# Performance work log

Hardware: AMD Instinct MI355X
Metric: run time of the kernel (lower is better)

## Reference

```python
import jax, jax.numpy as jnp
import numpy as np

EMBED_DIM = 1024
LN_EPS = 1e-5


def _layernorm(x, w, b):
    m = jnp.mean(x, axis=-1, keepdims=True)
    v = jnp.mean(jnp.square(x - m), axis=-1, keepdims=True)
    return (x - m) * jax.lax.rsqrt(v + LN_EPS) * w + b


def _attention(q, k, v, scale):
    # q: [b, sq, d], k/v: [b, sk, d]
    scores = jnp.einsum('bqd,bkd->bqk', q, k) * scale
    probs = jax.nn.softmax(scores, axis=-1)
    return jnp.einsum('bqk,bkd->bqd', probs, v)


def setup_inputs() -> dict:
    key = jax.random.key(0)
    ks = jax.random.split(key, 16)
    B, SQ, SK, D, H = 8, 577, 13271, EMBED_DIM, 4  # H=int(4.0) per source
    return {
        'input_features': jax.random.normal(ks[0], (B, SK, D), jnp.float32),
        'query_feature': jax.random.normal(ks[1], (B, SQ, D), jnp.float32),
        'norm1_w': jax.random.uniform(ks[2], (D,), jnp.float32, 0.5, 1.5),
        'norm1_b': jax.random.normal(ks[3], (D,), jnp.float32) * 0.1,
        'norm2_w': jax.random.uniform(ks[4], (D,), jnp.float32, 0.5, 1.5),
        'norm2_b': jax.random.normal(ks[5], (D,), jnp.float32) * 0.1,
        'norm3_w': jax.random.uniform(ks[6], (D,), jnp.float32, 0.5, 1.5),
        'norm3_b': jax.random.normal(ks[7], (D,), jnp.float32) * 0.1,
        'gamma1': jax.random.uniform(ks[8], (D,), jnp.float32, 0.5, 1.5),
        'gamma2': jax.random.uniform(ks[9], (D,), jnp.float32, 0.5, 1.5),
        'fc1_w': jax.random.normal(ks[10], (H, D), jnp.float32) * (1.0 / np.sqrt(D)),
        'fc1_b': jax.random.normal(ks[11], (H,), jnp.float32) * 0.01,
        'fc2_w': jax.random.normal(ks[12], (D, H), jnp.float32) * (1.0 / np.sqrt(H)),
        'fc2_b': jax.random.normal(ks[13], (D,), jnp.float32) * 0.01,
    }


def reference(input_features, query_feature, norm1_w, norm1_b, norm2_w, norm2_b,
              norm3_w, norm3_b, gamma1, gamma2, fc1_w, fc1_b, fc2_w, fc2_b):
    scale = EMBED_DIM ** (-0.5)
    norm_X = _layernorm(input_features, norm1_w, norm1_b)
    norm_F_L = _layernorm(query_feature, norm2_w, norm2_b)
    # cross attention: query = last-layer feats, key/value = concat of earlier layers
    attended = _attention(norm_F_L, norm_X, norm_X, scale)
    # MLP with exact-erf GELU (torch nn.GELU default), dropout=0 -> identity
    h = jax.nn.gelu(attended @ fc1_w.T + fc1_b, approximate=False)
    cross_attended = h @ fc2_w.T + fc2_b
    norm_cross = _layernorm(cross_attended, norm3_w, norm3_b)
    self_attended = _attention(norm_cross, norm_cross, norm_cross, scale)
    skip_connect = cross_attended + gamma1 * self_attended
    return norm_F_L + gamma2 * skip_connect
```

## Files before the change

### kernel.cpp

```cpp
#include <hip/hip_runtime.h>
#include <hip/hip_bf16.h>
#include <math.h>

typedef unsigned short u16;
typedef __attribute__((ext_vector_type(4))) unsigned short u16x4;
typedef __attribute__((ext_vector_type(8))) __bf16 bf16x8;
typedef __attribute__((ext_vector_type(4))) float fx4;

#define DEV __device__ __forceinline__

DEV u16 f2bf(float f) {
    unsigned u = __float_as_uint(f);
    u += 0x7fffu + ((u >> 16) & 1u);
    return (u16)(u >> 16);
}

DEV void async_load16(const void* g, void* l) {
    __builtin_amdgcn_global_load_lds(
        (const __attribute__((address_space(1))) void*)g,
        (__attribute__((address_space(3))) void*)l, 16, 0, 0);
}

DEV void block_reduce2(float& a, float& b) {
    #pragma unroll
    for (int o = 32; o; o >>= 1) { a += __shfl_xor(a, o); b += __shfl_xor(b, o); }
    __shared__ float sa[4], sb[4];
    const int lane = threadIdx.x & 63, wv = threadIdx.x >> 6;
    if (lane == 0) { sa[wv] = a; sb[wv] = b; }
    __syncthreads();
    a = sa[0] + sa[1] + sa[2] + sa[3];
    b = sb[0] + sb[1] + sb[2] + sb[3];
    __syncthreads();
}

DEV void xcd_swizzle3(int& bx, int& by, int& bz) {
    const int nx = gridDim.x, ny = gridDim.y;
    const int total = nx * ny * gridDim.z;
    const int lin = blockIdx.x + nx * (blockIdx.y + ny * blockIdx.z);
    const int cpx = total >> 3;
    const int swz = (lin & 7) * cpx + (lin >> 3);
    bx = swz % nx;
    const int r = swz / nx;
    by = r % ny;
    bz = r / ny;
}

__global__ __launch_bounds__(256) void ln_k(
    const float* __restrict__ in, int rows_real,
    const float* __restrict__ w, const float* __restrict__ bias,
    u16* __restrict__ out_bf, float* __restrict__ out_f32, float out_scale)
{
    const int r = blockIdx.x, b = blockIdx.y, tid = threadIdx.x;
    const int rows_pad = gridDim.x;
    const size_t orow = ((size_t)b * rows_pad + r) * 1024 + tid * 4;
    if (r >= rows_real) {
        u16x4 z = {0, 0, 0, 0};
        *(u16x4*)&out_bf[orow] = z;
        if (out_f32) { fx4 zf = {0.f, 0.f, 0.f, 0.f}; *(fx4*)&out_f32[orow] = zf; }
        return;
    }
    const size_t irow = ((size_t)b * rows_real + r) * 1024 + tid * 4;
    fx4 x = *(const fx4*)&in[irow];
    float s1 = x.x + x.y + x.z + x.w;
    float s2 = x.x * x.x + x.y * x.y + x.z * x.z + x.w * x.w;
    block_reduce2(s1, s2);
    float m = s1 * (1.0f / 1024.0f);
    float var = s2 * (1.0f / 1024.0f) - m * m;
    float rs = rsqrtf(var + 1e-5f);
    fx4 wv4 = *(const fx4*)&w[tid * 4];
    fx4 bv4 = *(const fx4*)&bias[tid * 4];
    fx4 y;
    y.x = (x.x - m) * rs * wv4.x + bv4.x;
    y.y = (x.y - m) * rs * wv4.y + bv4.y;
    y.z = (x.z - m) * rs * wv4.z + bv4.z;
    y.w = (x.w - m) * rs * wv4.w + bv4.w;
    u16x4 o = { f2bf(y.x * out_scale), f2bf(y.y * out_scale),
                f2bf(y.z * out_scale), f2bf(y.w * out_scale) };
    *(u16x4*)&out_bf[orow] = o;
    if (out_f32) *(fx4*)&out_f32[orow] = y;
}

template<bool ATOMIC>
DEV void gemm_body(
    const u16* __restrict__ Ab, const u16* __restrict__ Bb, float* __restrict__ Cb,
    int k_begin, int iters, int lda, int ldb, int ldc)
{
    __shared__ u16 lA[2][128 * 32];
    __shared__ u16 lB[2][128 * 32];
    const int lane = threadIdx.x & 63, wv = threadIdx.x >> 6;
    const int wm = (wv >> 1) * 64, wn = (wv & 1) * 64;
    const int frow = lane & 15, quad = lane >> 4;

    fx4 acc[4][4];
    #pragma unroll
    for (int i = 0; i < 4; ++i)
        #pragma unroll
        for (int j = 0; j < 4; ++j) { acc[i][j].x = 0; acc[i][j].y = 0; acc[i][j].z = 0; acc[i][j].w = 0; }

    const int c0 = wv * 64 + lane;
    const int r0a = c0 >> 2, s0 = (c0 & 3) * 8;
    const int c1 = 256 + c0;
    const int r1a = c1 >> 2, s1 = (c1 & 3) * 8;

    auto stage = [&](int buf, int it) {
        const int k0 = k_begin + it * 32;
        async_load16(Ab + (size_t)r0a * lda + k0 + s0, &lA[buf][(wv * 64) * 8]);
        async_load16(Ab + (size_t)r1a * lda + k0 + s1, &lA[buf][(256 + wv * 64) * 8]);
        async_load16(Bb + (size_t)r0a * ldb + k0 + s0, &lB[buf][(wv * 64) * 8]);
        async_load16(Bb + (size_t)r1a * ldb + k0 + s1, &lB[buf][(256 + wv * 64) * 8]);
    };

    stage(0, 0);
    __syncthreads();
    int cur = 0;
    for (int it = 0; it < iters; ++it) {
        if (it + 1 < iters) stage(cur ^ 1, it + 1);
        bf16x8 af[4], bfr[4];
        #pragma unroll
        for (int i = 0; i < 4; ++i) {
            af[i]  = *(const bf16x8*)&lA[cur][(wm + i * 16 + frow) * 32 + quad * 8];
            bfr[i] = *(const bf16x8*)&lB[cur][(wn + i * 16 + frow) * 32 + quad * 8];
        }
        #pragma unroll
        for (int mi = 0; mi < 4; ++mi)
            #pragma unroll
            for (int ni = 0; ni < 4; ++ni)
                acc[mi][ni] = __builtin_amdgcn_mfma_f32_16x16x32_bf16(af[mi], bfr[ni], acc[mi][ni], 0, 0, 0);
        __syncthreads();
        cur ^= 1;
    }

    #pragma unroll
    for (int mi = 0; mi < 4; ++mi) {
        #pragma unroll
        for (int r = 0; r < 4; ++r) {
            const int row = wm + mi * 16 + quad * 4 + r;
            #pragma unroll
            for (int ni = 0; ni < 4; ++ni) {
                const int col = wn + ni * 16 + frow;
                if (ATOMIC) atomicAdd(&Cb[(size_t)row * ldc + col], acc[mi][ni][r]);
                else        __builtin_nontemporal_store(acc[mi][ni][r], &Cb[(size_t)row * ldc + col]);
            }
        }
    }
}

__global__ __launch_bounds__(256) void gemm_bt(
    const u16* __restrict__ A, const u16* __restrict__ B, float* __restrict__ C,
    int K, int lda, int ldb, int ldc, long As, long Bs, long Cs)
{
    const int bz = blockIdx.z;
    const u16* Ab = A + (size_t)bz * As + (size_t)blockIdx.y * 128 * lda;
    const u16* Bb = B + (size_t)bz * Bs + (size_t)blockIdx.x * 128 * ldb;
    float* Cb = C + (size_t)bz * Cs + (size_t)blockIdx.y * 128 * ldc + (size_t)blockIdx.x * 128;
    gemm_body<false>(Ab, Bb, Cb, 0, K / 32, lda, ldb, ldc);
}

template<int NS>
__global__ __launch_bounds__(256) void gemm_bt_sk(
    const u16* __restrict__ A, const u16* __restrict__ B, float* __restrict__ C,
    int iters_per, int lda, int ldb, int ldc, long As, long Bs, long Cs)
{
    int bx, by, bzz;
    xcd_swizzle3(bx, by, bzz);
    const int bz = bzz / NS, sp = bzz % NS;
    const u16* Ab = A + (size_t)bz * As + (size_t)by * 128 * lda;
    const u16* Bb = B + (size_t)bz * Bs + (size_t)bx * 128 * ldb;
    float* Cb = C + (size_t)bz * Cs + (size_t)by * 128 * ldc + (size_t)bx * 128;
    gemm_body<true>(Ab, Bb, Cb, sp * iters_per * 32, iters_per, lda, ldb, ldc);
}

template<int EPT4>
__global__ __launch_bounds__(256) void softmax_k(
    const float* __restrict__ S, u16* __restrict__ P,
    int n_real, int n_pad, float scale, long Ss, long Ps)
{
    const int tid = threadIdx.x;
    const float* Sr = S + (size_t)blockIdx.y * Ss + (size_t)blockIdx.x * n_pad;
    u16* Pr = P + (size_t)blockIdx.y * Ps + (size_t)blockIdx.x * n_pad;
    fx4 v[EPT4];
    float mx = -INFINITY;
    #pragma unroll
    for (int i = 0; i < EPT4; ++i) {
        const int base = (i * 256 + tid) * 4;
        fx4 s;
        if (base < n_pad) s = *(const fx4*)&Sr[base];
        else { s.x = -INFINITY; s.y = -INFINITY; s.z = -INFINITY; s.w = -INFINITY; }
        s.x = (base + 0 < n_real) ? s.x * scale : -INFINITY;
        s.y = (base + 1 < n_real) ? s.y * scale : -INFINITY;
        s.z = (base + 2 < n_real) ? s.z * scale : -INFINITY;
        s.w = (base + 3 < n_real) ? s.w * scale : -INFINITY;
        v[i] = s;
        mx = fmaxf(mx, fmaxf(fmaxf(s.x, s.y), fmaxf(s.z, s.w)));
    }
    #pragma unroll
    for (int o = 32; o; o >>= 1) mx = fmaxf(mx, __shfl_xor(mx, o));
    __shared__ float sm[4];
    const int lane = tid & 63, wvi = tid >> 6;
    if (lane == 0) sm[wvi] = mx;
    __syncthreads();
    mx = fmaxf(fmaxf(sm[0], sm[1]), fmaxf(sm[2], sm[3]));
    __syncthreads();
    float sum = 0.f;
    #pragma unroll
    for (int i = 0; i < EPT4; ++i) {
        fx4 e;
        e.x = __expf(v[i].x - mx); e.y = __expf(v[i].y - mx);
        e.z = __expf(v[i].z - mx); e.w = __expf(v[i].w - mx);
        v[i] = e;
        sum += e.x + e.y + e.z + e.w;
    }
    #pragma unroll
    for (int o = 32; o; o >>= 1) sum += __shfl_xor(sum, o);
    if (lane == 0) sm[wvi] = sum;
    __syncthreads();
    sum = sm[0] + sm[1] + sm[2] + sm[3];
    const float inv = 1.0f / sum;
    #pragma unroll
    for (int i = 0; i < EPT4; ++i) {
        const int base = (i * 256 + tid) * 4;
        if (base < n_pad) {
            u16x4 o = { f2bf(v[i].x * inv), f2bf(v[i].y * inv),
                        f2bf(v[i].z * inv), f2bf(v[i].w * inv) };
            *(u16x4*)&Pr[base] = o;
        }
    }
}

__global__ __launch_bounds__(256) void transpose_k(
    const u16* __restrict__ in, u16* __restrict__ out,
    int in_rows, int in_cols, long is, long os)
{
    __shared__ u16 t[64][68];
    const int b = blockIdx.z;
    const u16* I = in + (size_t)b * is;
    u16* O = out + (size_t)b * os;
    const int c0 = blockIdx.x * 64, r0 = blockIdx.y * 64;
    const int cx = threadIdx.x & 15, ry = threadIdx.x >> 4;
    u16x4 a[4];
    #pragma unroll
    for (int k = 0; k < 4; ++k)
        a[k] = *(const u16x4*)&I[(size_t)(r0 + 4 * ry + k) * in_cols + c0 + 4 * cx];
    #pragma unroll
    for (int e = 0; e < 4; ++e) {
        u16x4 o = { a[0][e], a[1][e], a[2][e], a[3][e] };
        *(u16x4*)&t[4 * cx + e][4 * ry] = o;
    }
    __syncthreads();
    #pragma unroll
    for (int k = 0; k < 4; ++k) {
        const int oc = 4 * ry + k;
        *(u16x4*)&O[(size_t)(c0 + oc) * in_rows + r0 + 4 * cx] =
            *(const u16x4*)&t[oc][4 * cx];
    }
}

__global__ __launch_bounds__(256) void mlp_ln_k(
    const float* __restrict__ att, const float* __restrict__ w1, const float* __restrict__ b1,
    const float* __restrict__ w2, const float* __restrict__ b2,
    const float* __restrict__ w3, const float* __restrict__ b3,
    float* __restrict__ ca, u16* __restrict__ nc, int rows_real)
{
    const int q = blockIdx.x, b = blockIdx.y, tid = threadIdx.x;
    const size_t row = ((size_t)b * gridDim.x + q) * 1024 + tid * 4;
    if (q >= rows_real) {
        fx4 zf = {0.f, 0.f, 0.f, 0.f}; u16x4 z = {0, 0, 0, 0};
        *(fx4*)&ca[row] = zf;
        *(u16x4*)&nc[row] = z;
        return;
    }
    fx4 x = *(const fx4*)&att[row];
    float p[4];
    #pragma unroll
    for (int j = 0; j < 4; ++j) {
        fx4 wj = *(const fx4*)&w1[j * 1024 + tid * 4];
        p[j] = x.x * wj.x + x.y * wj.y + x.z * wj.z + x.w * wj.w;
        #pragma unroll
        for (int o = 32; o; o >>= 1) p[j] += __shfl_xor(p[j], o);
    }
    __shared__ float sh[4][4];
    const int lane = tid & 63, wvi = tid >> 6;
    if (lane == 0) { sh[wvi][0] = p[0]; sh[wvi][1] = p[1]; sh[wvi][2] = p[2]; sh[wvi][3] = p[3]; }
    __syncthreads();
    float h[4];
    #pragma unroll
    for (int j = 0; j < 4; ++j) {
        float s = sh[0][j] + sh[1][j] + sh[2][j] + sh[3][j] + b1[j];
        h[j] = 0.5f * s * (1.0f + erff(s * 0.70710678118f));
    }
    float v[4]; float s1 = 0.f, s2 = 0.f;
    #pragma unroll
    for (int e = 0; e < 4; ++e) {
        const int d = tid * 4 + e;
        fx4 wd = *(const fx4*)&w2[d * 4];
        float t = h[0] * wd.x + h[1] * wd.y + h[2] * wd.z + h[3] * wd.w + b2[d];
        v[e] = t; s1 += t; s2 += t * t;
    }
    block_reduce2(s1, s2);
    const float m = s1 * (1.0f / 1024.0f);
    const float var = s2 * (1.0f / 1024.0f) - m * m;
    const float rs = rsqrtf(var + 1e-5f);
    fx4 cav = {v[0], v[1], v[2], v[3]};
    *(fx4*)&ca[row] = cav;
    fx4 w3v = *(const fx4*)&w3[tid * 4], b3v = *(const fx4*)&b3[tid * 4];
    u16x4 o = { f2bf((v[0] - m) * rs * w3v.x + b3v.x), f2bf((v[1] - m) * rs * w3v.y + b3v.y),
                f2bf((v[2] - m) * rs * w3v.z + b3v.z), f2bf((v[3] - m) * rs * w3v.w + b3v.w) };
    *(u16x4*)&nc[row] = o;
}

__global__ __launch_bounds__(256) void final_k(
    const float* __restrict__ nF, const float* __restrict__ ca,
    const float* __restrict__ att2, const float* __restrict__ g1,
    const float* __restrict__ g2, float* __restrict__ out, int sq, int sqp)
{
    const int q = blockIdx.x, b = blockIdx.y, tid = threadIdx.x;
    const size_t wrow = ((size_t)b * sqp + q) * 1024 + tid * 4;
    const size_t orow = ((size_t)b * sq + q) * 1024 + tid * 4;
    fx4 nf = *(const fx4*)&nF[wrow];
    fx4 c  = *(const fx4*)&ca[wrow];
    fx4 a2 = *(const fx4*)&att2[wrow];
    fx4 G1 = *(const fx4*)&g1[tid * 4];
    fx4 G2 = *(const fx4*)&g2[tid * 4];
    fx4 r;
    r.x = nf.x + G2.x * (c.x + G1.x * a2.x);
    r.y = nf.y + G2.y * (c.y + G1.y * a2.y);
    r.z = nf.z + G2.z * (c.z + G1.z * a2.z);
    r.w = nf.w + G2.w * (c.w + G1.w * a2.w);
    *(fx4*)&out[orow] = r;
}

extern "C" void kernel_launch(void* const* d_in, const int* in_sizes, int n_in,
                              void* d_out, int out_size, void* d_ws, size_t ws_size,
                              hipStream_t stream) {
    const float* x_in = (const float*)d_in[0];
    const float* q_in = (const float*)d_in[1];
    const float* n1w = (const float*)d_in[2];
    const float* n1b = (const float*)d_in[3];
    const float* n2w = (const float*)d_in[4];
    const float* n2b = (const float*)d_in[5];
    const float* n3w = (const float*)d_in[6];
    const float* n3b = (const float*)d_in[7];
    const float* g1  = (const float*)d_in[8];
    const float* g2  = (const float*)d_in[9];
    const float* w1  = (const float*)d_in[10];
    const float* b1  = (const float*)d_in[11];
    const float* w2  = (const float*)d_in[12];
    const float* b2  = (const float*)d_in[13];
    float* out = (float*)d_out;

    const int B = 8, SQ = 577, SK = 13271, D = 1024;
    const int SQP = 640, SKP = 13312;
    const float scale = 0.03125f;

    char* ws = (char*)d_ws;
    size_t off = 0;
    auto alloc = [&](size_t n) { size_t o = off; off = (off + n + 255) & ~(size_t)255; return o; };
    u16*   Xn   = (u16*)  (ws + alloc((size_t)B * SKP * D * 2));
    u16*   Xt   = (u16*)  (ws + alloc((size_t)B * D * SKP * 2));
    u16*   Qb   = (u16*)  (ws + alloc((size_t)B * SQP * D * 2));
    float* nF   = (float*)(ws + alloc((size_t)B * SQP * D * 4));
    u16*   P    = (u16*)  (ws + alloc((size_t)B * SQP * SKP * 2));
    float* att  = (float*)(ws + alloc((size_t)B * SQP * D * 4));
    float* CA   = (float*)(ws + alloc((size_t)B * SQP * D * 4));
    u16*   NC   = (u16*)  (ws + alloc((size_t)B * SQP * D * 2));
    u16*   NCt  = (u16*)  (ws + alloc((size_t)B * D * SQP * 2));
    float* S2   = (float*)(ws + alloc((size_t)B * SQP * SQP * 4));
    u16*   P2   = (u16*)  (ws + alloc((size_t)B * SQP * SQP * 2));
    float* att2 = (float*)(ws + alloc((size_t)B * SQP * D * 4));
    const size_t perS1 = (size_t)SQP * SKP * 4;
    size_t room = (ws_size > off) ? (ws_size - off) / perS1 : 1;
    int g = (int)(room < 1 ? 1 : (room > 8 ? 8 : room));
    float* S1 = (float*)(ws + off);
    (void)in_sizes; (void)n_in; (void)out_size;

    ln_k<<<dim3(SKP, B), 256, 0, stream>>>(x_in, SK, n1w, n1b, Xn, nullptr, 1.0f);
    ln_k<<<dim3(SQP, B), 256, 0, stream>>>(q_in, SQ, n2w, n2b, Qb, nF, scale);

    transpose_k<<<dim3(D / 64, SKP / 64, B), 256, 0, stream>>>(
        Xn, Xt, SKP, D, (long)SKP * D, (long)SKP * D);

    for (int b = 0; b < B; b += g) {
        const int nb = (B - b) < g ? (B - b) : g;
        gemm_bt<<<dim3(SKP / 128, SQP / 128, nb), 256, 0, stream>>>(
            Qb + (size_t)b * SQP * D, Xn + (size_t)b * SKP * D, S1,
            D, D, D, SKP, (long)SQP * D, (long)SKP * D, (long)SQP * SKP);
        softmax_k<13><<<dim3(SQP, nb), 256, 0, stream>>>(
            S1, P + (size_t)b * SQP * SKP, SK, SKP, 1.0f,
            (long)SQP * SKP, (long)SQP * SKP);
    }

    hipMemsetAsync(att, 0, (size_t)B * SQP * D * 4, stream);
    gemm_bt_sk<4><<<dim3(D / 128, SQP / 128, B * 4), 256, 0, stream>>>(
        P, Xt, att, 104, SKP, SKP, D,
        (long)SQP * SKP, (long)D * SKP, (long)SQP * D);

    mlp_ln_k<<<dim3(SQP, B), 256, 0, stream>>>(att, w1, b1, w2, b2, n3w, n3b, CA, NC, SQ);

    transpose_k<<<dim3(D / 64, SQP / 64, B), 256, 0, stream>>>(
        NC, NCt, SQP, D, (long)SQP * D, (long)SQP * D);
    hipMemsetAsync(S2, 0, (size_t)B * SQP * SQP * 4, stream);
    gemm_bt_sk<2><<<dim3(SQP / 128, SQP / 128, B * 2), 256, 0, stream>>>(
        NC, NC, S2, 16, D, D, SQP,
        (long)SQP * D, (long)SQP * D, (long)SQP * SQP);
    softmax_k<1><<<dim3(SQP, B), 256, 0, stream>>>(
        S2, P2, SQ, SQP, scale, (long)SQP * SQP, (long)SQP * SQP);
    hipMemsetAsync(att2, 0, (size_t)B * SQP * D * 4, stream);
    gemm_bt_sk<4><<<dim3(D / 128, SQP / 128, B * 4), 256, 0, stream>>>(
        P2, NCt, att2, 5, SQP, SQP, D,
        (long)SQP * SQP, (long)D * SQP, (long)SQP * D);

    final_k<<<dim3(SQ, B), 256, 0, stream>>>(nF, CA, att2, g1, g2, out, SQ, SQP);
}
```

Baseline: 1.347 ms.

## Use 256x256-tile 512-thread GEMM with 64-wide K stages for cross-attention

Adds a new GEMM kernel with 256x256 output tiles, 8 waves, 64-wide K steps and quarter-tile phased double buffering that interleaves async LDS loads with MFMA work. It replaces the 128x128 GEMMs for the QK^T scores and the split-K P·V product, which now uses 8 splits. Rows past the padded M are clamped on load and masked on store. The larger tiles raise data reuse and cut global and LDS traffic. In exchange they add register pressure, waste more work on padded rows (3 tiles of 256 cover 640 rows), and bring more atomic traffic from the larger split-K.

```diff
diff --git a/kernel.cpp b/kernel.cpp
--- a/kernel.cpp
+++ b/kernel.cpp
@@ -37,6 +37,7 @@
     const int nx = gridDim.x, ny = gridDim.y;
     const int total = nx * ny * gridDim.z;
     const int lin = blockIdx.x + nx * (blockIdx.y + ny * blockIdx.z);
+    if (total & 7) { bx = blockIdx.x; by = blockIdx.y; bz = blockIdx.z; return; }
     const int cpx = total >> 3;
     const int swz = (lin & 7) * cpx + (lin >> 3);
     bx = swz % nx;
@@ -145,17 +146,6 @@
     }
 }
 
-__global__ __launch_bounds__(256) void gemm_bt(
-    const u16* __restrict__ A, const u16* __restrict__ B, float* __restrict__ C,
-    int K, int lda, int ldb, int ldc, long As, long Bs, long Cs)
-{
-    const int bz = blockIdx.z;
-    const u16* Ab = A + (size_t)bz * As + (size_t)blockIdx.y * 128 * lda;
-    const u16* Bb = B + (size_t)bz * Bs + (size_t)blockIdx.x * 128 * ldb;
-    float* Cb = C + (size_t)bz * Cs + (size_t)blockIdx.y * 128 * ldc + (size_t)blockIdx.x * 128;
-    gemm_body<false>(Ab, Bb, Cb, 0, K / 32, lda, ldb, ldc);
-}
-
 template<int NS>
 __global__ __launch_bounds__(256) void gemm_bt_sk(
     const u16* __restrict__ A, const u16* __restrict__ B, float* __restrict__ C,
@@ -168,6 +158,146 @@
     const u16* Bb = B + (size_t)bz * Bs + (size_t)bx * 128 * ldb;
     float* Cb = C + (size_t)bz * Cs + (size_t)by * 128 * ldc + (size_t)bx * 128;
     gemm_body<true>(Ab, Bb, Cb, sp * iters_per * 32, iters_per, lda, ldb, ldc);
+}
+
+template<bool ATOMIC>
+DEV void gemm256_body(
+    const u16* __restrict__ A, const u16* __restrict__ B, float* __restrict__ C,
+    int k_begin, int NT, int lda, int ldb, int ldc, int bx, int by, int Mreal)
+{
+    __shared__ u16 lds[2][4][8192];
+    const int tid = threadIdx.x;
+    const int lane = tid & 63, wid = tid >> 6;
+    const int wr = wid >> 2, wc = wid & 3;
+    const int frow = lane & 15, quad = lane >> 4;
+    const int sw = (frow & 7) << 4;
+    const int csrc = ((lane & 7) ^ ((lane >> 3) & 7)) * 8;
+    const int by256 = by * 256, bx256 = bx * 256;
+    const int mclamp = Mreal - 1;
+
+    fx4 acc[8][4];
+    #pragma unroll
+    for (int i = 0; i < 8; ++i)
+        #pragma unroll
+        for (int j = 0; j < 4; ++j) { acc[i][j].x = 0; acc[i][j].y = 0; acc[i][j].z = 0; acc[i][j].w = 0; }
+
+    auto stageA = [&](int buf, int half, int ktile) {
+        const int kcol = k_begin + ktile * 64;
+        #pragma unroll
+        for (int j = 0; j < 2; ++j) {
+            int grow = by256 + half * 128 + (wid * 2 + j) * 8 + (lane >> 3);
+            if (grow > mclamp) grow = mclamp;
+            async_load16(A + (size_t)grow * lda + kcol + csrc,
+                         &lds[buf][half][(wid * 2 + j) * 512]);
+        }
+    };
+    auto stageB = [&](int buf, int half, int ktile) {
+        const int kcol = k_begin + ktile * 64;
+        #pragma unroll
+        for (int j = 0; j < 2; ++j) {
+            const int grow = bx256 + half * 128 + (wid * 2 + j) * 8 + (lane >> 3);
+            async_load16(B + (size_t)grow * ldb + kcol + csrc,
+                         &lds[buf][2 + half][(wid * 2 + j) * 512]);
+        }
+    };
+
+#define DO_PHASE(MQ, NQ, STAGE_STMT, WAITN)                                              \
+    {                                                                                    \
+        STAGE_STMT;                                                                      \
+        __builtin_amdgcn_sched_barrier(0);                                               \
+        asm volatile("s_waitcnt vmcnt(" #WAITN ")" ::: "memory");                        \
+        __builtin_amdgcn_s_barrier();                                                    \
+        __builtin_amdgcn_sched_barrier(0);                                               \
+        const char* pa = (const char*)&lds[cur][MQ][0];                                  \
+        const char* pb = (const char*)&lds[cur][2 + NQ][0];                              \
+        bf16x8 av[4][2], bv[2][2];                                                       \
+        _Pragma("unroll")                                                                \
+        for (int f = 0; f < 4; ++f) {                                                    \
+            const int row = wr * 64 + f * 16 + frow;                                     \
+            _Pragma("unroll")                                                            \
+            for (int ks = 0; ks < 2; ++ks)                                               \
+                av[f][ks] = *(const bf16x8*)(pa + row * 128 + ((((ks * 4 + quad) << 4)) ^ sw)); \
+        }                                                                                \
+        _Pragma("unroll")                                                                \
+        for (int gg = 0; gg < 2; ++gg) {                                                 \
+            const int col = wc * 32 + gg * 16 + frow;                                    \
+            _Pragma("unroll")                                                            \
+            for (int ks = 0; ks < 2; ++ks)                                               \
+                bv[gg][ks] = *(const bf16x8*)(pb + col * 128 + ((((ks * 4 + quad) << 4)) ^ sw)); \
+        }                                                                                \
+        __builtin_amdgcn_s_setprio(1);                                                   \
+        _Pragma("unroll")                                                                \
+        for (int f = 0; f < 4; ++f)                                                      \
+            _Pragma("unroll")                                                            \
+            for (int gg = 0; gg < 2; ++gg)                                               \
+                _Pragma("unroll")                                                        \
+                for (int ks = 0; ks < 2; ++ks)                                           \
+                    acc[MQ * 4 + f][NQ * 2 + gg] = __builtin_amdgcn_mfma_f32_16x16x32_bf16( \
+                        av[f][ks], bv[gg][ks], acc[MQ * 4 + f][NQ * 2 + gg], 0, 0, 0);   \
+        __builtin_amdgcn_s_setprio(0);                                                   \
+    }
+
+    stageA(0, 0, 0);
+    stageB(0, 0, 0);
+    stageB(0, 1, 0);
+    stageA(0, 1, 0);
+    stageA(1, 0, 1);
+
+    int cur = 0;
+    for (int t = 0; t <= NT - 2; ++t) {
+        const int nxt = cur ^ 1;
+        DO_PHASE(0, 0, stageB(nxt, 0, t + 1), 8)
+        DO_PHASE(0, 1, stageB(nxt, 1, t + 1), 8)
+        DO_PHASE(1, 0, stageA(nxt, 1, t + 1), 8)
+        DO_PHASE(1, 1, if (t + 2 < NT) stageA(cur, 0, t + 2), 8)
+        cur = nxt;
+    }
+    DO_PHASE(0, 0, (void)0, 4)
+    DO_PHASE(0, 1, (void)0, 2)
+    DO_PHASE(1, 0, (void)0, 0)
+    DO_PHASE(1, 1, (void)0, 0)
+#undef DO_PHASE
+
+    #pragma unroll
+    for (int mf = 0; mf < 8; ++mf) {
+        const int rowb = (mf >> 2) * 128 + wr * 64 + (mf & 3) * 16 + quad * 4;
+        #pragma unroll
+        for (int r = 0; r < 4; ++r) {
+            const int grow = by256 + rowb + r;
+            if (grow < Mreal) {
+                #pragma unroll
+                for (int nf = 0; nf < 4; ++nf) {
+                    const int gcol = bx256 + (nf >> 1) * 128 + wc * 32 + (nf & 1) * 16 + frow;
+                    if (ATOMIC) atomicAdd(&C[(size_t)grow * ldc + gcol], acc[mf][nf][r]);
+                    else __builtin_nontemporal_store(acc[mf][nf][r], &C[(size_t)grow * ldc + gcol]);
+                }
+            }
+        }
+    }
+}
+
+__global__ __launch_bounds__(512, 2) void gemm256_qk(
+    const u16* __restrict__ A, const u16* __restrict__ B, float* __restrict__ C,
+    int NT, int lda, int ldb, int ldc, long As, long Bs, long Cs, int Mreal)
+{
+    const int lin = blockIdx.x + gridDim.x * (blockIdx.y + gridDim.y * blockIdx.z);
+    const int per_bx = gridDim.y * gridDim.z;
+    const int bx = lin / per_bx, rem = lin % per_bx;
+    const int by = rem % gridDim.y, bz = rem / gridDim.y;
+    gemm256_body<false>(A + (size_t)bz * As, B + (size_t)bz * Bs, C + (size_t)bz * Cs,
+                        0, NT, lda, ldb, ldc, bx, by, Mreal);
+}
+
+template<int NS>
+__global__ __launch_bounds__(512, 2) void gemm256_sk(
+    const u16* __restrict__ A, const u16* __restrict__ B, float* __restrict__ C,
+    int NT_per, int lda, int ldb, int ldc, long As, long Bs, long Cs, int Mreal)
+{
+    int bx, by, bzz;
+    xcd_swizzle3(bx, by, bzz);
+    const int bz = bzz / NS, sp = bzz % NS;
+    gemm256_body<true>(A + (size_t)bz * As, B + (size_t)bz * Bs, C + (size_t)bz * Cs,
+                       sp * NT_per * 64, NT_per, lda, ldb, ldc, bx, by, Mreal);
 }
 
 template<int EPT4>
@@ -381,18 +511,18 @@
 
     for (int b = 0; b < B; b += g) {
         const int nb = (B - b) < g ? (B - b) : g;
-        gemm_bt<<<dim3(SKP / 128, SQP / 128, nb), 256, 0, stream>>>(
+        gemm256_qk<<<dim3(SKP / 256, 3, nb), 512, 0, stream>>>(
             Qb + (size_t)b * SQP * D, Xn + (size_t)b * SKP * D, S1,
-            D, D, D, SKP, (long)SQP * D, (long)SKP * D, (long)SQP * SKP);
+            D / 64, D, D, SKP, (long)SQP * D, (long)SKP * D, (long)SQP * SKP, SQP);
         softmax_k<13><<<dim3(SQP, nb), 256, 0, stream>>>(
             S1, P + (size_t)b * SQP * SKP, SK, SKP, 1.0f,
             (long)SQP * SKP, (long)SQP * SKP);
     }
 
     hipMemsetAsync(att, 0, (size_t)B * SQP * D * 4, stream);
-    gemm_bt_sk<4><<<dim3(D / 128, SQP / 128, B * 4), 256, 0, stream>>>(
-        P, Xt, att, 104, SKP, SKP, D,
-        (long)SQP * SKP, (long)D * SKP, (long)SQP * D);
+    gemm256_sk<8><<<dim3(D / 256, 3, B * 8), 512, 0, stream>>>(
+        P, Xt, att, (SKP / 64) / 8, SKP, SKP, D,
+        (long)SQP * SKP, (long)D * SKP, (long)SQP * D, SQP);
 
     mlp_ln_k<<<dim3(SQP, B), 256, 0, stream>>>(att, w1, b1, w2, b2, n3w, n3b, CA, NC, SQ);
 
```

New measurement: 1.321 ms. 2.0% less time.
